# Optimization experiments

Measured on AMD Instinct MI355X. Metric: run time of the kernel, lower is better.

## Reference

```python
import jax, jax.numpy as jnp
import numpy as np

D_OUT = 8192
D_IN = 8192
BA = 64  # block size for A (output side)
BB = 64  # block size for B (input side)
NA = D_OUT // BA
NB = D_IN // BB


def setup_inputs() -> dict:
    key = jax.random.key(0)
    k1, k2, k3 = jax.random.split(key, 3)
    # W plays the role of naive_compression_module.reconstruct(): dense d_out x d_in
    W = jax.random.normal(k1, (D_OUT, D_IN), dtype=jnp.float32)
    # Block-diagonal A (d_out x d_out) stored as stack of diagonal blocks [nA, bA, bA]
    A_blocks = jax.random.normal(k2, (NA, BA, BA), dtype=jnp.float32)
    # Block-diagonal B (d_in x d_in) stored as [nB, bB, bB]
    B_blocks = jax.random.normal(k3, (NB, BB, BB), dtype=jnp.float32)
    return {"W": W, "A_blocks": A_blocks, "B_blocks": B_blocks}


def reference(W, A_blocks, B_blocks):
    # out = A @ W @ B with A, B block-diagonal; skip the zero off-diagonal blocks.
    nA, bA, _ = A_blocks.shape
    nB, bB, _ = B_blocks.shape
    d_out = nA * bA
    d_in = nB * bB
    # Left multiply: each A block acts on its own bA-row slab of W.
    # [nA, bA, bA] @ [nA, bA, d_in] -> [nA, bA, d_in]
    AW = jnp.einsum('nab,nbj->naj', A_blocks, W.reshape(nA, bA, d_in)).reshape(d_out, d_in)
    # Right multiply: each B block acts on its own bB-column slab.
    # [d_out, nB, bB] @ [nB, bB, bB] -> [d_out, nB, bB]
    out = jnp.einsum('inb,nbc->inc', AW.reshape(d_out, nB, bB), B_blocks).reshape(d_out, d_in)
    return out
```

## Files before the change

### kernel.cpp

```cpp
#include <hip/hip_runtime.h>
#include <hip/hip_bf16.h>


#define D 8192
#define BS 64
#define GITER 8
#define LSTR 72

typedef __bf16  bf16x8 __attribute__((ext_vector_type(8)));
typedef float   f32x4  __attribute__((ext_vector_type(4)));

__device__ __forceinline__ unsigned short f2bf(float f) {
    union { float f; unsigned u; } v; v.f = f;
    unsigned r = v.u + 0x7FFFu + ((v.u >> 16) & 1u);
    return (unsigned short)(r >> 16);
}

__device__ __forceinline__ unsigned pkbf(float lo, float hi) {
    union { __hip_bfloat162 h; unsigned u; } c;
    c.h = __float22bfloat162_rn(make_float2(lo, hi));
    return c.u;
}

__device__ __forceinline__ bf16x8 mkfrag(f32x4 lo, f32x4 hi) {
    union { unsigned u[4]; bf16x8 v; } r;
    r.u[0] = pkbf(lo[0], lo[1]);
    r.u[1] = pkbf(lo[2], lo[3]);
    r.u[2] = pkbf(hi[0], hi[1]);
    r.u[3] = pkbf(hi[2], hi[3]);
    return r.v;
}

__device__ __forceinline__ void lds_barrier() {
    asm volatile("s_waitcnt lgkmcnt(0)" ::: "memory");
    __builtin_amdgcn_s_barrier();
    asm volatile("" ::: "memory");
}

__global__ __launch_bounds__(256, 4) void bcl_kernel(
    const float* __restrict__ W,
    const float* __restrict__ Ab,
    const float* __restrict__ Bb,
    float* __restrict__ out)
{
    __shared__ __align__(16) unsigned short Bt[BS * LSTR];
    __shared__ __align__(16) unsigned short Tt[2][BS * LSTR];

    const int t  = threadIdx.x;
    const int b  = blockIdx.x;
    const int a0 = blockIdx.y * GITER;

    const int lane = t & 63;
    const int wv   = t >> 6;
    const int l16  = lane & 15;
    const int quad = lane >> 4;
    const int m0   = wv * 16;
    const int frow = m0 + l16;
    const int kq   = quad * 8;

    const float* Wp = W   + (size_t)(a0 * BS + frow) * D + b * BS + kq;
    const float* Ap = Ab  + (size_t)a0 * BS * BS + frow * BS + kq;
    float*       Op = out + (size_t)(a0 * BS + m0 + quad * 4) * D + b * BS + l16;

    f32x4 w0 = __builtin_nontemporal_load((const f32x4*)(Wp + 0));
    f32x4 w1 = __builtin_nontemporal_load((const f32x4*)(Wp + 4));
    f32x4 w2 = __builtin_nontemporal_load((const f32x4*)(Wp + 32));
    f32x4 w3 = __builtin_nontemporal_load((const f32x4*)(Wp + 36));
    f32x4 av0 = *(const f32x4*)(Ap + 0);
    f32x4 av1 = *(const f32x4*)(Ap + 4);
    f32x4 av2 = *(const f32x4*)(Ap + 32);
    f32x4 av3 = *(const f32x4*)(Ap + 36);

    {
        const float* Bg = Bb + (size_t)b * BS * BS;
        const int r0 = t >> 4;
        const int c4 = (t & 15) << 2;
        #pragma unroll
        for (int i = 0; i < 4; ++i) {
            const int k = i * 16 + r0;
            f32x4 v = *(const f32x4*)(Bg + k * BS + c4);
            Bt[(c4 + 0) * LSTR + k] = f2bf(v[0]);
            Bt[(c4 + 1) * LSTR + k] = f2bf(v[1]);
            Bt[(c4 + 2) * LSTR + k] = f2bf(v[2]);
            Bt[(c4 + 3) * LSTR + k] = f2bf(v[3]);
        }
    }
    lds_barrier();

    bf16x8 btf[4][2];
    #pragma unroll
    for (int j = 0; j < 4; ++j) {
        btf[j][0] = *(const bf16x8*)&Bt[(j * 16 + l16) * LSTR + kq];
        btf[j][1] = *(const bf16x8*)&Bt[(j * 16 + l16) * LSTR + 32 + kq];
    }

    int buf = 0;
    #pragma unroll 1
    for (int i = 0; i < GITER; ++i) {
        bf16x8 waf0 = mkfrag(w0, w1);
        bf16x8 waf1 = mkfrag(w2, w3);
        bf16x8 aaf0 = mkfrag(av0, av1);
        bf16x8 aaf1 = mkfrag(av2, av3);

        if (i + 1 < GITER) {
            const float* Wn = Wp + (size_t)(i + 1) * BS * D;
            const float* An = Ap + (i + 1) * BS * BS;
            w0 = __builtin_nontemporal_load((const f32x4*)(Wn + 0));
            w1 = __builtin_nontemporal_load((const f32x4*)(Wn + 4));
            w2 = __builtin_nontemporal_load((const f32x4*)(Wn + 32));
            w3 = __builtin_nontemporal_load((const f32x4*)(Wn + 36));
            av0 = *(const f32x4*)(An + 0);
            av1 = *(const f32x4*)(An + 4);
            av2 = *(const f32x4*)(An + 32);
            av3 = *(const f32x4*)(An + 36);
        }

        f32x4 acc1[4] = {};
        #pragma unroll
        for (int j = 0; j < 4; ++j)
            acc1[j] = __builtin_amdgcn_mfma_f32_16x16x32_bf16(waf0, btf[j][0], acc1[j], 0, 0, 0);
        #pragma unroll
        for (int j = 0; j < 4; ++j)
            acc1[j] = __builtin_amdgcn_mfma_f32_16x16x32_bf16(waf1, btf[j][1], acc1[j], 0, 0, 0);

        unsigned short* Tb = Tt[buf];
        #pragma unroll
        for (int j = 0; j < 4; ++j) {
            uint2 p;
            p.x = pkbf(acc1[j][0], acc1[j][1]);
            p.y = pkbf(acc1[j][2], acc1[j][3]);
            *(uint2*)&Tb[(j * 16 + l16) * LSTR + m0 + quad * 4] = p;
        }
        lds_barrier();

        f32x4 acc2[4] = {};
        #pragma unroll
        for (int j = 0; j < 4; ++j) {
            bf16x8 tf = *(const bf16x8*)&Tb[(j * 16 + l16) * LSTR + kq];
            acc2[j] = __builtin_amdgcn_mfma_f32_16x16x32_bf16(aaf0, tf, acc2[j], 0, 0, 0);
        }
        #pragma unroll
        for (int j = 0; j < 4; ++j) {
            bf16x8 tf = *(const bf16x8*)&Tb[(j * 16 + l16) * LSTR + 32 + kq];
            acc2[j] = __builtin_amdgcn_mfma_f32_16x16x32_bf16(aaf1, tf, acc2[j], 0, 0, 0);
        }

        float* Or = Op + (size_t)i * BS * D;
        #pragma unroll
        for (int j = 0; j < 4; ++j) {
            #pragma unroll
            for (int r = 0; r < 4; ++r)
                __builtin_nontemporal_store(acc2[j][r], Or + (size_t)r * D + j * 16);
        }

        buf ^= 1;
    }
}

extern "C" void kernel_launch(void* const* d_in, const int* in_sizes, int n_in,
                              void* d_out, int out_size, void* d_ws, size_t ws_size,
                              hipStream_t stream) {
    const float* W = (const float*)d_in[0];
    const float* A = (const float*)d_in[1];
    const float* B = (const float*)d_in[2];
    float* o = (float*)d_out;
    dim3 grid(D / BS, D / BS / GITER);
    bcl_kernel<<<grid, 256, 0, stream>>>(W, A, B, o);
}
```

Measured before the change: 461.9 us.

## Transpose second-stage MFMA so output rows are written as 16-byte vector stores

The second GEMM now uses T as the A operand and the A block as the B operand, read from a new LDS tile. This yields the transposed product, so each lane holds four contiguous output columns and can write them with one f32x4 nontemporal store instead of four scalar stores. The A block is staged row-wise through LDS, and the T buffer is single-buffered with a barrier at the top of each loop iteration. In exchange, the B fragments are re-read from LDS every iteration instead of staying in registers, and there is more LDS traffic plus an extra barrier per iteration.

```diff
diff --git a/kernel.cpp b/kernel.cpp
--- a/kernel.cpp
+++ b/kernel.cpp
@@ -9,12 +9,6 @@
 
 typedef __bf16  bf16x8 __attribute__((ext_vector_type(8)));
 typedef float   f32x4  __attribute__((ext_vector_type(4)));
-
-__device__ __forceinline__ unsigned short f2bf(float f) {
-    union { float f; unsigned u; } v; v.f = f;
-    unsigned r = v.u + 0x7FFFu + ((v.u >> 16) & 1u);
-    return (unsigned short)(r >> 16);
-}
 
 __device__ __forceinline__ unsigned pkbf(float lo, float hi) {
     union { __hip_bfloat162 h; unsigned u; } c;
@@ -44,7 +38,8 @@
     float* __restrict__ out)
 {
     __shared__ __align__(16) unsigned short Bt[BS * LSTR];
-    __shared__ __align__(16) unsigned short Tt[2][BS * LSTR];
+    __shared__ __align__(16) unsigned short Tt[BS * LSTR];
+    __shared__ __align__(16) unsigned short Al[BS * LSTR];
 
     const int t  = threadIdx.x;
     const int b  = blockIdx.x;
@@ -55,52 +50,55 @@
     const int l16  = lane & 15;
     const int quad = lane >> 4;
     const int m0   = wv * 16;
-    const int frow = m0 + l16;
     const int kq   = quad * 8;
 
-    const float* Wp = W   + (size_t)(a0 * BS + frow) * D + b * BS + kq;
-    const float* Ap = Ab  + (size_t)a0 * BS * BS + frow * BS + kq;
-    float*       Op = out + (size_t)(a0 * BS + m0 + quad * 4) * D + b * BS + l16;
+    const int r0 = t >> 4;
+    const int c4 = (t & 15) << 2;
+
+    const float* Wp = W   + (size_t)(a0 * BS + m0 + l16) * D + b * BS + kq;
+    const float* Ap = Ab  + (size_t)a0 * BS * BS + r0 * BS + c4;
+    float*       Op = out + (size_t)(a0 * BS + l16) * D + b * BS + m0 + quad * 4;
 
     f32x4 w0 = __builtin_nontemporal_load((const f32x4*)(Wp + 0));
     f32x4 w1 = __builtin_nontemporal_load((const f32x4*)(Wp + 4));
     f32x4 w2 = __builtin_nontemporal_load((const f32x4*)(Wp + 32));
     f32x4 w3 = __builtin_nontemporal_load((const f32x4*)(Wp + 36));
-    f32x4 av0 = *(const f32x4*)(Ap + 0);
-    f32x4 av1 = *(const f32x4*)(Ap + 4);
-    f32x4 av2 = *(const f32x4*)(Ap + 32);
-    f32x4 av3 = *(const f32x4*)(Ap + 36);
+    f32x4 ar0 = *(const f32x4*)(Ap + 0 * 16 * BS);
+    f32x4 ar1 = *(const f32x4*)(Ap + 1 * 16 * BS);
+    f32x4 ar2 = *(const f32x4*)(Ap + 2 * 16 * BS);
+    f32x4 ar3 = *(const f32x4*)(Ap + 3 * 16 * BS);
 
     {
         const float* Bg = Bb + (size_t)b * BS * BS;
-        const int r0 = t >> 4;
-        const int c4 = (t & 15) << 2;
         #pragma unroll
         for (int i = 0; i < 4; ++i) {
             const int k = i * 16 + r0;
             f32x4 v = *(const f32x4*)(Bg + k * BS + c4);
-            Bt[(c4 + 0) * LSTR + k] = f2bf(v[0]);
-            Bt[(c4 + 1) * LSTR + k] = f2bf(v[1]);
-            Bt[(c4 + 2) * LSTR + k] = f2bf(v[2]);
-            Bt[(c4 + 3) * LSTR + k] = f2bf(v[3]);
+            Bt[(c4 + 0) * LSTR + k] = (unsigned short)(pkbf(v[0], v[0]) & 0xFFFFu);
+            Bt[(c4 + 1) * LSTR + k] = (unsigned short)(pkbf(v[1], v[1]) & 0xFFFFu);
+            Bt[(c4 + 2) * LSTR + k] = (unsigned short)(pkbf(v[2], v[2]) & 0xFFFFu);
+            Bt[(c4 + 3) * LSTR + k] = (unsigned short)(pkbf(v[3], v[3]) & 0xFFFFu);
         }
     }
-    lds_barrier();
 
-    bf16x8 btf[4][2];
-    #pragma unroll
-    for (int j = 0; j < 4; ++j) {
-        btf[j][0] = *(const bf16x8*)&Bt[(j * 16 + l16) * LSTR + kq];
-        btf[j][1] = *(const bf16x8*)&Bt[(j * 16 + l16) * LSTR + 32 + kq];
-    }
-
-    int buf = 0;
     #pragma unroll 1
     for (int i = 0; i < GITER; ++i) {
+        lds_barrier();
+
+        {
+            uint2 p;
+            p.x = pkbf(ar0[0], ar0[1]); p.y = pkbf(ar0[2], ar0[3]);
+            *(uint2*)&Al[(0 * 16 + r0) * LSTR + c4] = p;
+            p.x = pkbf(ar1[0], ar1[1]); p.y = pkbf(ar1[2], ar1[3]);
+            *(uint2*)&Al[(1 * 16 + r0) * LSTR + c4] = p;
+            p.x = pkbf(ar2[0], ar2[1]); p.y = pkbf(ar2[2], ar2[3]);
+            *(uint2*)&Al[(2 * 16 + r0) * LSTR + c4] = p;
+            p.x = pkbf(ar3[0], ar3[1]); p.y = pkbf(ar3[2], ar3[3]);
+            *(uint2*)&Al[(3 * 16 + r0) * LSTR + c4] = p;
+        }
+
         bf16x8 waf0 = mkfrag(w0, w1);
         bf16x8 waf1 = mkfrag(w2, w3);
-        bf16x8 aaf0 = mkfrag(av0, av1);
-        bf16x8 aaf1 = mkfrag(av2, av3);
 
         if (i + 1 < GITER) {
             const float* Wn = Wp + (size_t)(i + 1) * BS * D;
@@ -109,51 +107,51 @@
             w1 = __builtin_nontemporal_load((const f32x4*)(Wn + 4));
             w2 = __builtin_nontemporal_load((const f32x4*)(Wn + 32));
             w3 = __builtin_nontemporal_load((const f32x4*)(Wn + 36));
-            av0 = *(const f32x4*)(An + 0);
-            av1 = *(const f32x4*)(An + 4);
-            av2 = *(const f32x4*)(An + 32);
-            av3 = *(const f32x4*)(An + 36);
+            ar0 = *(const f32x4*)(An + 0 * 16 * BS);
+            ar1 = *(const f32x4*)(An + 1 * 16 * BS);
+            ar2 = *(const f32x4*)(An + 2 * 16 * BS);
+            ar3 = *(const f32x4*)(An + 3 * 16 * BS);
         }
 
         f32x4 acc1[4] = {};
         #pragma unroll
-        for (int j = 0; j < 4; ++j)
-            acc1[j] = __builtin_amdgcn_mfma_f32_16x16x32_bf16(waf0, btf[j][0], acc1[j], 0, 0, 0);
-        #pragma unroll
-        for (int j = 0; j < 4; ++j)
-            acc1[j] = __builtin_amdgcn_mfma_f32_16x16x32_bf16(waf1, btf[j][1], acc1[j], 0, 0, 0);
+        for (int s = 0; s < 2; ++s) {
+            const int k0 = s * 32 + kq;
+            const bf16x8 wa = s ? waf1 : waf0;
+            #pragma unroll
+            for (int j = 0; j < 4; ++j) {
+                bf16x8 bf = *(const bf16x8*)&Bt[(j * 16 + l16) * LSTR + k0];
+                acc1[j] = __builtin_amdgcn_mfma_f32_16x16x32_bf16(wa, bf, acc1[j], 0, 0, 0);
+            }
+        }
 
-        unsigned short* Tb = Tt[buf];
         #pragma unroll
         for (int j = 0; j < 4; ++j) {
             uint2 p;
             p.x = pkbf(acc1[j][0], acc1[j][1]);
             p.y = pkbf(acc1[j][2], acc1[j][3]);
-            *(uint2*)&Tb[(j * 16 + l16) * LSTR + m0 + quad * 4] = p;
+            *(uint2*)&Tt[(j * 16 + l16) * LSTR + m0 + quad * 4] = p;
         }
         lds_barrier();
 
         f32x4 acc2[4] = {};
         #pragma unroll
-        for (int j = 0; j < 4; ++j) {
-            bf16x8 tf = *(const bf16x8*)&Tb[(j * 16 + l16) * LSTR + kq];
-            acc2[j] = __builtin_amdgcn_mfma_f32_16x16x32_bf16(aaf0, tf, acc2[j], 0, 0, 0);
-        }
-        #pragma unroll
-        for (int j = 0; j < 4; ++j) {
-            bf16x8 tf = *(const bf16x8*)&Tb[(j * 16 + l16) * LSTR + 32 + kq];
-            acc2[j] = __builtin_amdgcn_mfma_f32_16x16x32_bf16(aaf1, tf, acc2[j], 0, 0, 0);
+        for (int s = 0; s < 2; ++s) {
+            const int k0 = s * 32 + kq;
+            bf16x8 ta = *(const bf16x8*)&Tt[(m0 + l16) * LSTR + k0];
+            #pragma unroll
+            for (int j = 0; j < 4; ++j) {
+                bf16x8 ab = *(const bf16x8*)&Al[(j * 16 + l16) * LSTR + k0];
+                acc2[j] = __builtin_amdgcn_mfma_f32_16x16x32_bf16(ta, ab, acc2[j], 0, 0, 0);
+            }
         }
 
         float* Or = Op + (size_t)i * BS * D;
         #pragma unroll
         for (int j = 0; j < 4; ++j) {
-            #pragma unroll
-            for (int r = 0; r < 4; ++r)
-                __builtin_nontemporal_store(acc2[j][r], Or + (size_t)r * D + j * 16);
+            f32x4 v = acc2[j];
+            __builtin_nontemporal_store(v, (f32x4*)(Or + (size_t)(j * 16) * D));
         }
-
-        buf ^= 1;
     }
 }
 
```

After: 463.3 us. About the same (+0.3%).
